# Performance work log

Measured on AMD Instinct MI355X. Metric: run time of the kernel, lower is better.

The kernel has to match this reference:

```python
import jax, jax.numpy as jnp
import numpy as np
from math import factorial, sqrt

LMAX = 2
NB = 32
NRBF = 20
CUTOFF = 5.0
N_ATOMS = 20000
N_EDGES = 400000
T = 2
M = (LMAX + 1) ** 2
LIDX = np.repeat(np.arange(LMAX + 1), 2 * np.arange(LMAX + 1) + 1)  # l of each flat (l,m) index


def _cg_complex(j1, m1, j2, m2, j3, m3):
    # Racah formula for complex-SH Clebsch-Gordan coefficients
    if m3 != m1 + m2 or j3 < abs(j1 - j2) or j3 > j1 + j2:
        return 0.0
    f = factorial
    pref = sqrt((2 * j3 + 1) * f(j1 + j2 - j3) * f(j1 - j2 + j3) * f(-j1 + j2 + j3) / f(j1 + j2 + j3 + 1))
    pref *= sqrt(f(j1 + m1) * f(j1 - m1) * f(j2 + m2) * f(j2 - m2) * f(j3 + m3) * f(j3 - m3))
    kmin = max(0, j2 - j3 - m1, j1 + m2 - j3)
    kmax = min(j1 + j2 - j3, j1 - m1, j2 + m2)
    s = 0.0
    for k in range(kmin, kmax + 1):
        s += (-1) ** k / (f(k) * f(j1 + j2 - j3 - k) * f(j1 - m1 - k) * f(j2 + m2 - k) * f(j3 - j2 + m1 + k) * f(j3 - j1 - m2 + k))
    return pref * s


def _u_matrix(l):
    # real-SH = U @ complex-SH (rows: real m from -l..l, cols: complex m')
    U = np.zeros((2 * l + 1, 2 * l + 1), dtype=np.complex128)
    for m in range(-l, l + 1):
        if m == 0:
            U[l, l] = 1.0
        elif m > 0:
            U[l + m, l + m] = (-1) ** m / sqrt(2)
            U[l + m, l - m] = 1.0 / sqrt(2)
        else:
            mu = -m
            U[l + m, l + m] = 1j / sqrt(2)
            U[l + m, l - m] = -1j * (-1) ** mu / sqrt(2)
    return U


def _build_cg_rsh(lmax):
    # CG coefficients in the real-SH basis, parity invariant (odd l1+l2+l3 blocks zero)
    cg = np.zeros((M, M, M), dtype=np.float64)
    Us = [_u_matrix(l) for l in range(lmax + 1)]
    for l1 in range(lmax + 1):
        for l2 in range(lmax + 1):
            for l3 in range(lmax + 1):
                if (l1 + l2 + l3) % 2 == 1 or l3 < abs(l1 - l2) or l3 > l1 + l2:
                    continue
                Cc = np.zeros((2 * l1 + 1, 2 * l2 + 1, 2 * l3 + 1), dtype=np.complex128)
                for i, m1 in enumerate(range(-l1, l1 + 1)):
                    for j, m2 in enumerate(range(-l2, l2 + 1)):
                        m3 = m1 + m2
                        if abs(m3) <= l3:
                            Cc[i, j, l3 + m3] = _cg_complex(l1, m1, l2, m2, l3, m3)
                R = np.einsum('ai,bj,ck,ijk->abc', Us[l1], Us[l2], np.conj(Us[l3]), Cc)
                cg[l1 * l1:(l1 + 1) ** 2, l2 * l2:(l2 + 1) ** 2, l3 * l3:(l3 + 1) ** 2] = np.real(R)
    return cg.astype(np.float32)


CG = jnp.asarray(_build_cg_rsh(LMAX))   # [9, 9, 9]
LIDX_J = jnp.asarray(LIDX)


def _rsh(dirs):
    # real spherical harmonics up to l=2 on unit vectors, flat (l,m) order -> [P, 9]
    x, y, z = dirs[:, 0], dirs[:, 1], dirs[:, 2]
    c1 = 0.4886025119029199
    c2 = 1.0925484305920792
    return jnp.stack([
        jnp.full_like(x, 0.28209479177387814),
        c1 * y, c1 * z, c1 * x,
        c2 * x * y, c2 * y * z,
        0.31539156525252005 * (3.0 * z * z - 1.0),
        c2 * x * z,
        0.5462742152960396 * (x * x - y * y),
    ], axis=1)


def _forward(atomic_numbers, r_ij, idx_i, idx_j, emb, Wf, bf, Wm1, Wm2, Wm3, Wg, bg):
    d = jnp.linalg.norm(r_ij, axis=1)                      # [P]
    Y = _rsh(r_ij / d[:, None])                            # [P, 9]
    offsets = jnp.linspace(0.0, CUTOFF, NRBF)
    width = CUTOFF / (NRBF - 1)
    radial = jnp.exp(-0.5 / width ** 2 * (d[:, None] - offsets) ** 2)   # GaussianRBF [P, NRBF]
    fcut = jnp.where(d < CUTOFF, 0.5 * (jnp.cos(d * jnp.pi / CUTOFF) + 1.0), 0.0)  # CosineCutoff
    x0 = emb[atomic_numbers]                               # nuclear embedding [N, NB]
    x = jnp.concatenate([x0[:, None, :], jnp.zeros((x0.shape[0], M - 1, NB), x0.dtype)], axis=1)  # scalar2rsh
    for t in range(T):
        # SO3Convolution: per-edge radial filter per output degree l, cutoff gated
        Wl = ((radial @ Wf[t].T + bf[t]) * fcut[:, None]).reshape(-1, LMAX + 1, NB)
        xj = x[idx_j]                                      # gather neighbors [P, 9, NB]
        tbc = jnp.einsum('pa,abc->pbc', Y, CG)             # contract Y_ij with CG
        yij = jnp.einsum('pbc,pbn->pcn', tbc, xj) * Wl[:, LIDX_J, :]
        dx = jax.ops.segment_sum(yij, idx_i, num_segments=x.shape[0], indices_are_sorted=True)
        ddx = jnp.einsum('xcn,kn->xck', dx, Wm1[t])        # mixing1 (no bias)
        dx = dx + jnp.einsum('abc,xan,xbn->xcn', CG, dx, ddx)  # SO3TensorProduct
        dx = jnp.einsum('xcn,kn->xck', dx, Wm2[t])         # mixing2
        h = jax.nn.sigmoid((dx[:, 0, :] @ Wg[t].T + bg[t]).reshape(-1, LMAX + 1, NB))
        dx = dx * h[:, LIDX_J, :]                          # SO3ParametricGatedNonlinearity
        dx = jnp.einsum('xcn,kn->xck', dx, Wm3[t])         # mixing3
        x = x + dx
    return x                                               # multipole representation [N, 9, NB]


def setup_inputs():
    key = jax.random.key(0)
    ks = jax.random.split(key, 12)
    return {
        'atomic_numbers': jax.random.randint(ks[0], (N_ATOMS,), 1, 100),
        'r_ij': jax.random.normal(ks[1], (N_EDGES, 3), jnp.float32),
        'idx_i': jnp.sort(jax.random.randint(ks[2], (N_EDGES,), 0, N_ATOMS)),
        'idx_j': jax.random.randint(ks[3], (N_EDGES,), 0, N_ATOMS),
        'emb': jax.random.normal(ks[4], (101, NB), jnp.float32).at[0].set(0.0),
        'Wf': jax.random.normal(ks[5], (T, (LMAX + 1) * NB, NRBF), jnp.float32) / sqrt(NRBF),
        'bf': jnp.zeros((T, (LMAX + 1) * NB), jnp.float32),
        'Wm1': jax.random.normal(ks[6], (T, NB, NB), jnp.float32) / sqrt(NB),
        'Wm2': jax.random.normal(ks[7], (T, NB, NB), jnp.float32) / sqrt(NB),
        'Wm3': jax.random.normal(ks[8], (T, NB, NB), jnp.float32) / sqrt(NB),
        'Wg': jax.random.normal(ks[9], (T, (LMAX + 1) * NB, NB), jnp.float32) / sqrt(NB),
        'bg': jnp.zeros((T, (LMAX + 1) * NB), jnp.float32),
    }


def reference(atomic_numbers, r_ij, idx_i, idx_j, emb, Wf, bf, Wm1, Wm2, Wm3, Wg, bg):
    return _forward(atomic_numbers, r_ij, idx_i, idx_j, emb, Wf, bf, Wm1, Wm2, Wm3, Wg, bg)
```

## Files before the change

kernel.cpp:

```cpp
#include <hip/hip_runtime.h>

#define CHUNK 16

constexpr double CFACT[8] = {1.,1.,2.,6.,24.,120.,720.,5040.};

constexpr double csqrt(double x){
  if (x <= 0.0) return 0.0;
  double s = 1.0;
  while (x > 4.0)  { x *= 0.25; s *= 2.0; }
  while (x < 0.25) { x *= 4.0;  s *= 0.5; }
  double g = 1.0;
  for (int i=0;i<10;i++) g = 0.5*(g + x/g);
  return s*g;
}

constexpr double cg_complex(int j1,int m1,int j2,int m2,int j3,int m3){
  if (m3 != m1+m2 || j3 < (j1>j2?j1-j2:j2-j1) || j3 > j1+j2) return 0.0;
  double pref = csqrt((2.0*j3+1.0)*CFACT[j1+j2-j3]*CFACT[j1-j2+j3]*CFACT[-j1+j2+j3]/CFACT[j1+j2+j3+1]);
  pref *= csqrt(CFACT[j1+m1]*CFACT[j1-m1]*CFACT[j2+m2]*CFACT[j2-m2]*CFACT[j3+m3]*CFACT[j3-m3]);
  int kmin = 0;
  if (j2-j3-m1 > kmin) kmin = j2-j3-m1;
  if (j1+m2-j3 > kmin) kmin = j1+m2-j3;
  int kmax = j1+j2-j3;
  if (j1-m1 < kmax) kmax = j1-m1;
  if (j2+m2 < kmax) kmax = j2+m2;
  double s = 0.0;
  for (int k=kmin;k<=kmax;++k){
    double t = 1.0/(CFACT[k]*CFACT[j1+j2-j3-k]*CFACT[j1-m1-k]*CFACT[j2+m2-k]*CFACT[j3-j2+m1+k]*CFACT[j3-j1-m2+k]);
    s += (k&1)? -t : t;
  }
  return pref*s;
}

struct UR { int n; int mc[2]; double re[2]; double im[2]; };
constexpr UR u_row(int m){
  UR u{}; const double is2 = 0.70710678118654752440;
  if (m==0){ u.n=1; u.mc[0]=0; u.re[0]=1.0; u.im[0]=0.0; u.mc[1]=0; u.re[1]=0.0; u.im[1]=0.0; }
  else if (m>0){ u.n=2; u.mc[0]=m;  u.re[0]=((m&1)? -is2:is2); u.im[0]=0.0;
                        u.mc[1]=-m; u.re[1]=is2;               u.im[1]=0.0; }
  else { int mu=-m; u.n=2; u.mc[0]=m;  u.re[0]=0.0; u.im[0]=is2;
                           u.mc[1]=mu; u.re[1]=0.0; u.im[1]=((mu&1)? is2:-is2); }
  return u;
}

struct CGTab { float v[9][9][9]; };
constexpr CGTab build_cg(){
  CGTab g{};
  double cc[9][9][9] = {};
  for (int a=0;a<9;a++){
    int l1 = (a==0)?0:((a<4)?1:2); int m1 = a - (l1*l1+l1);
    for (int b=0;b<9;b++){
      int l2 = (b==0)?0:((b<4)?1:2); int m2 = b - (l2*l2+l2);
      int m3 = m1+m2;
      for (int l3=0;l3<=2;l3++){
        if (m3 < -l3 || m3 > l3) continue;
        cc[a][b][l3*l3+l3+m3] = cg_complex(l1,m1,l2,m2,l3,m3);
      }
    }
  }
  for (int l1=0;l1<=2;l1++) for (int l2=0;l2<=2;l2++) for (int l3=0;l3<=2;l3++){
    if (((l1+l2+l3)&1)==1) continue;
    int dl = (l1>l2)?(l1-l2):(l2-l1);
    if (l3 < dl || l3 > l1+l2) continue;
    for (int m1=-l1;m1<=l1;m1++) for (int m2=-l2;m2<=l2;m2++) for (int m3=-l3;m3<=l3;m3++){
      UR ua = u_row(m1), ub = u_row(m2), uc = u_row(m3);
      double acc = 0.0;
      for (int i=0;i<ua.n;i++) for (int j=0;j<ub.n;j++){
        double zr = ua.re[i]*ub.re[j] - ua.im[i]*ub.im[j];
        double zi = ua.re[i]*ub.im[j] + ua.im[i]*ub.re[j];
        for (int k=0;k<uc.n;k++){
          double rp = zr*uc.re[k] + zi*uc.im[k];
          if (rp != 0.0)
            acc += rp * cc[l1*l1+l1+ua.mc[i]][l2*l2+l2+ub.mc[j]][l3*l3+l3+uc.mc[k]];
        }
      }
      g.v[l1*l1+l1+m1][l2*l2+l2+m2][l3*l3+l3+m3] = (float)acc;
    }
  }
  return g;
}
constexpr CGTab CGT = build_cg();

__global__ void init_x_kernel(const int* __restrict__ Z, const float* __restrict__ emb,
                              float4* __restrict__ x4, float4* __restrict__ dx4, int n_atoms){
  int i = blockIdx.x*blockDim.x + threadIdx.x;
  if (i >= n_atoms*72) return;
  int atom = i/72, rem = i - atom*72;
  float4 v = make_float4(0.f,0.f,0.f,0.f);
  if (rem < 8) v = reinterpret_cast<const float4*>(emb)[Z[atom]*8 + rem];
  x4[i] = v;
  dx4[i] = make_float4(0.f,0.f,0.f,0.f);
}

template<bool FIRST>
__global__ __launch_bounds__(256) void edge_kernel(
    const float* __restrict__ r_ij, const int* __restrict__ idx_i, const int* __restrict__ idx_j,
    const float* __restrict__ x, const float* __restrict__ Wf_t, const float* __restrict__ bf_t,
    float* __restrict__ dx, int n_edges)
{
  __shared__ __align__(16) float rbs[8][32];
  int tid = threadIdx.x;
  int g = tid >> 5, lane = tid & 31;
  int base = (blockIdx.x*8 + g)*CHUNK;
  if (base >= n_edges) return;
  const int nend = n_edges;

  float wfr[3][20]; float bfl[3];
  #pragma unroll
  for (int l=0;l<3;l++){
    const float* rp = Wf_t + (l*32+lane)*20;
    #pragma unroll
    for (int q=0;q<5;q++){
      float4 v4 = *reinterpret_cast<const float4*>(rp + q*4);
      wfr[l][q*4+0]=v4.x; wfr[l][q*4+1]=v4.y; wfr[l][q*4+2]=v4.z; wfr[l][q*4+3]=v4.w;
    }
    bfl[l] = bf_t[l*32+lane];
  }

  const float STEP  = 5.0f/19.0f;
  const float ALPHA = -0.5f/(STEP*STEP);
  float myoff = (float)lane * STEP;

  float racc[9];
  #pragma unroll
  for (int c=0;c<9;c++) racc[c]=0.f;
  int cur_i = -1;

  float xj[9]; float xj0 = 0.f;
  {
    int j0 = idx_j[base];
    const float* xp = x + j0*288 + lane;
    if (FIRST){ xj0 = xp[0]; }
    else {
      #pragma unroll
      for (int b=0;b<9;b++) xj[b] = xp[b*32];
    }
  }
  int e1 = (base+1 <= nend-1) ? base+1 : nend-1;
  int j_next = idx_j[e1];

  #pragma unroll 2
  for (int k=0;k<CHUNK;k++){
    int e = base + k;
    if (e >= nend) break;

    float xjn[9]; float xjn0 = 0.f;
    {
      const float* xp = x + j_next*288 + lane;
      if (FIRST){ xjn0 = xp[0]; }
      else {
        #pragma unroll
        for (int b=0;b<9;b++) xjn[b] = xp[b*32];
      }
    }
    int en2 = (e+2 <= nend-1) ? e+2 : nend-1;
    int j_n2 = idx_j[en2];

    int   ii = idx_i[e];
    float rx = r_ij[3*e+0], ry = r_ij[3*e+1], rz = r_ij[3*e+2];

    float d2 = fmaf(rx,rx,fmaf(ry,ry,rz*rz));
    float inv = __frsqrt_rn(d2);
    float dd = d2*inv;
    float X = rx*inv, Yv = ry*inv, Zv = rz*inv;
    const float c1 = 0.4886025119029199f, c2 = 1.0925484305920792f;
    float Y[9];
    Y[0]=0.28209479177387814f; Y[1]=c1*Yv; Y[2]=c1*Zv; Y[3]=c1*X;
    Y[4]=c2*X*Yv; Y[5]=c2*Yv*Zv; Y[6]=0.31539156525252005f*(3.f*Zv*Zv-1.f);
    Y[7]=c2*X*Zv; Y[8]=0.5462742152960396f*(X*X-Yv*Yv);

    float dtl = dd - myoff;
    float rbl = __expf(ALPHA*dtl*dtl);
    if (lane < 20) rbs[g][lane] = rbl;
    __builtin_amdgcn_wave_barrier();
    float rbv[20];
    {
      const float4* rb4 = reinterpret_cast<const float4*>(&rbs[g][0]);
      #pragma unroll
      for (int q=0;q<5;q++){
        float4 v4 = rb4[q];
        rbv[4*q+0]=v4.x; rbv[4*q+1]=v4.y; rbv[4*q+2]=v4.z; rbv[4*q+3]=v4.w;
      }
    }
    float wl0=bfl[0], wl1=bfl[1], wl2=bfl[2];
    #pragma unroll
    for (int r=0;r<20;r++){
      wl0 = fmaf(rbv[r], wfr[0][r], wl0);
      wl1 = fmaf(rbv[r], wfr[1][r], wl1);
      wl2 = fmaf(rbv[r], wfr[2][r], wl2);
    }
    float fc = (dd < 5.0f) ? 0.5f*(__cosf(dd*0.6283185307179586f)+1.0f) : 0.0f;
    wl0*=fc; wl1*=fc; wl2*=fc;

    if (ii != cur_i){
      if (cur_i >= 0){
        float* dp = dx + cur_i*288 + lane;
        #pragma unroll
        for (int c=0;c<9;c++){ atomicAdd(dp + c*32, racc[c]); racc[c]=0.f; }
      }
      cur_i = ii;
    }

    if (FIRST){
      racc[0] = fmaf(wl0, Y[0]*xj0, racc[0]);
      #pragma unroll
      for (int c=1;c<4;c++) racc[c] = fmaf(wl1, Y[c]*xj0, racc[c]);
      #pragma unroll
      for (int c=4;c<9;c++) racc[c] = fmaf(wl2, Y[c]*xj0, racc[c]);
    } else {
      float yv[9];
      #pragma unroll
      for (int c=0;c<9;c++) yv[c]=0.f;
      #pragma unroll
      for (int a=0;a<9;a++){
        #pragma unroll
        for (int b=0;b<9;b++){
          bool any = false;
          #pragma unroll
          for (int c=0;c<9;c++) any = any | (CGT.v[a][b][c] != 0.f);
          if (any){
            float p = Y[a]*xj[b];
            #pragma unroll
            for (int c=0;c<9;c++){
              if (CGT.v[a][b][c] != 0.f) yv[c] = fmaf(CGT.v[a][b][c], p, yv[c]);
            }
          }
        }
      }
      racc[0] = fmaf(wl0, yv[0], racc[0]);
      #pragma unroll
      for (int c=1;c<4;c++) racc[c] = fmaf(wl1, yv[c], racc[c]);
      #pragma unroll
      for (int c=4;c<9;c++) racc[c] = fmaf(wl2, yv[c], racc[c]);
    }

    j_next = j_n2;
    if (FIRST){ xj0 = xjn0; }
    else {
      #pragma unroll
      for (int b=0;b<9;b++) xj[b] = xjn[b];
    }
  }
  if (cur_i >= 0){
    float* dp = dx + cur_i*288 + lane;
    #pragma unroll
    for (int c=0;c<9;c++) atomicAdd(dp + c*32, racc[c]);
  }
}

__global__ __launch_bounds__(256) void atom_kernel(
    float* __restrict__ x, float* __restrict__ dxg,
    const float* __restrict__ Wm1_t, const float* __restrict__ Wm2_t, const float* __restrict__ Wm3_t,
    const float* __restrict__ Wg_t, const float* __restrict__ bg_t, int n_atoms)
{
  __shared__ __align__(16) float tile[8][288];
  int tid = threadIdx.x;
  int g = tid>>5, k = tid&31;
  int atom = blockIdx.x*8 + g;
  if (atom >= n_atoms) return;
  float* tg = &tile[g][0];
  const float4* t4 = reinterpret_cast<const float4*>(tg);

  float* dp = dxg + atom*288 + k;
  float v[9];
  #pragma unroll
  for (int c=0;c<9;c++){ v[c]=dp[c*32]; tg[c*32+k]=v[c]; dp[c*32]=0.f; }

  float wr[32];
  {
    const float4* w4 = reinterpret_cast<const float4*>(Wm1_t + k*32);
    #pragma unroll
    for (int q=0;q<8;q++){ float4 a=w4[q]; wr[4*q]=a.x; wr[4*q+1]=a.y; wr[4*q+2]=a.z; wr[4*q+3]=a.w; }
  }
  float u[9];
  #pragma unroll
  for (int c=0;c<9;c++){
    float s=0.f;
    #pragma unroll
    for (int q=0;q<8;q++){
      float4 tv = t4[c*8+q];
      s = fmaf(tv.x, wr[4*q+0], s); s = fmaf(tv.y, wr[4*q+1], s);
      s = fmaf(tv.z, wr[4*q+2], s); s = fmaf(tv.w, wr[4*q+3], s);
    }
    u[c]=s;
  }

  float w[9];
  #pragma unroll
  for (int c=0;c<9;c++) w[c]=v[c];
  #pragma unroll
  for (int a=0;a<9;a++){
    #pragma unroll
    for (int b=0;b<9;b++){
      bool any = false;
      #pragma unroll
      for (int c=0;c<9;c++) any = any | (CGT.v[a][b][c] != 0.f);
      if (any){
        float p = v[a]*u[b];
        #pragma unroll
        for (int c=0;c<9;c++){
          if (CGT.v[a][b][c] != 0.f) w[c] = fmaf(CGT.v[a][b][c], p, w[c]);
        }
      }
    }
  }

  #pragma unroll
  for (int c=0;c<9;c++) tg[c*32+k]=w[c];
  {
    const float4* w4 = reinterpret_cast<const float4*>(Wm2_t + k*32);
    #pragma unroll
    for (int q=0;q<8;q++){ float4 a=w4[q]; wr[4*q]=a.x; wr[4*q+1]=a.y; wr[4*q+2]=a.z; wr[4*q+3]=a.w; }
  }
  float p[9];
  #pragma unroll
  for (int c=0;c<9;c++){
    float s=0.f;
    #pragma unroll
    for (int q=0;q<8;q++){
      float4 tv = t4[c*8+q];
      s = fmaf(tv.x, wr[4*q+0], s); s = fmaf(tv.y, wr[4*q+1], s);
      s = fmaf(tv.z, wr[4*q+2], s); s = fmaf(tv.w, wr[4*q+3], s);
    }
    p[c]=s;
  }

  tg[k] = p[0];
  float s0=bg_t[k], s1=bg_t[32+k], s2=bg_t[64+k];
  {
    const float4* wg0 = reinterpret_cast<const float4*>(Wg_t + (     k)*32);
    const float4* wg1 = reinterpret_cast<const float4*>(Wg_t + (32 + k)*32);
    const float4* wg2 = reinterpret_cast<const float4*>(Wg_t + (64 + k)*32);
    #pragma unroll
    for (int q=0;q<8;q++){
      float4 tv = t4[q];
      float4 a0 = wg0[q], a1 = wg1[q], a2 = wg2[q];
      s0 = fmaf(tv.x,a0.x,s0); s0 = fmaf(tv.y,a0.y,s0); s0 = fmaf(tv.z,a0.z,s0); s0 = fmaf(tv.w,a0.w,s0);
      s1 = fmaf(tv.x,a1.x,s1); s1 = fmaf(tv.y,a1.y,s1); s1 = fmaf(tv.z,a1.z,s1); s1 = fmaf(tv.w,a1.w,s1);
      s2 = fmaf(tv.x,a2.x,s2); s2 = fmaf(tv.y,a2.y,s2); s2 = fmaf(tv.z,a2.z,s2); s2 = fmaf(tv.w,a2.w,s2);
    }
  }
  float h0 = 1.f/(1.f+__expf(-s0));
  float h1 = 1.f/(1.f+__expf(-s1));
  float h2 = 1.f/(1.f+__expf(-s2));

  float q9[9];
  q9[0]=p[0]*h0;
  #pragma unroll
  for (int c=1;c<4;c++) q9[c]=p[c]*h1;
  #pragma unroll
  for (int c=4;c<9;c++) q9[c]=p[c]*h2;

  #pragma unroll
  for (int c=0;c<9;c++) tg[c*32+k]=q9[c];
  {
    const float4* w4 = reinterpret_cast<const float4*>(Wm3_t + k*32);
    #pragma unroll
    for (int q=0;q<8;q++){ float4 a=w4[q]; wr[4*q]=a.x; wr[4*q+1]=a.y; wr[4*q+2]=a.z; wr[4*q+3]=a.w; }
  }
  float* xo = x + atom*288 + k;
  #pragma unroll
  for (int c=0;c<9;c++){
    float s=0.f;
    #pragma unroll
    for (int q=0;q<8;q++){
      float4 tv = t4[c*8+q];
      s = fmaf(tv.x, wr[4*q+0], s); s = fmaf(tv.y, wr[4*q+1], s);
      s = fmaf(tv.z, wr[4*q+2], s); s = fmaf(tv.w, wr[4*q+3], s);
    }
    xo[c*32] += s;
  }
}

extern "C" void kernel_launch(void* const* d_in, const int* in_sizes, int n_in,
                              void* d_out, int out_size, void* d_ws, size_t ws_size,
                              hipStream_t stream)
{
  const int*   Z    = (const int*)d_in[0];
  const float* r_ij = (const float*)d_in[1];
  const int*   idxi = (const int*)d_in[2];
  const int*   idxj = (const int*)d_in[3];
  const float* emb  = (const float*)d_in[4];
  const float* Wf   = (const float*)d_in[5];
  const float* bf   = (const float*)d_in[6];
  const float* Wm1  = (const float*)d_in[7];
  const float* Wm2  = (const float*)d_in[8];
  const float* Wm3  = (const float*)d_in[9];
  const float* Wg   = (const float*)d_in[10];
  const float* bg   = (const float*)d_in[11];
  int n_atoms = in_sizes[0];
  int n_edges = in_sizes[1]/3;

  float* x  = (float*)d_out;
  float* dx = (float*)d_ws;

  init_x_kernel<<<(n_atoms*72+255)/256,256,0,stream>>>(Z, emb, (float4*)x, (float4*)dx, n_atoms);

  int eblocks = (n_edges + 8*CHUNK - 1)/(8*CHUNK);
  int ablocks = (n_atoms + 7)/8;

  edge_kernel<true><<<eblocks,256,0,stream>>>(r_ij, idxi, idxj, x, Wf, bf, dx, n_edges);
  atom_kernel<<<ablocks,256,0,stream>>>(x, dx, Wm1, Wm2, Wm3, Wg, bg, n_atoms);

  edge_kernel<false><<<eblocks,256,0,stream>>>(r_ij, idxi, idxj, x,
                                        Wf + 96*20, bf + 96, dx, n_edges);
  atom_kernel<<<ablocks,256,0,stream>>>(x, dx,
                                        Wm1 + 1024, Wm2 + 1024, Wm3 + 1024,
                                        Wg + 96*32, bg + 96, n_atoms);
}
```

Measured before the change: 385.0 us.

## Use packed FMA for radial filter and deepen FIRST-layer gather prefetch

Stores the radial filter weights as float2 pairs and computes the three filter dot products with packed elementwise FMAs, intended to lower to v_pk_fma_f32 and halve the FMA instruction count. In the FIRST edge kernel, the x_j gather prefetch is extended to two edges ahead to hide more load latency. The distance is now computed with sqrtf instead of d2*rsqrt, which costs an extra instruction but avoids a NaN for zero-length vectors. Pairwise accumulation reorders the float sums slightly, and the deeper prefetch keeps more registers live.

```diff
diff --git a/kernel.cpp b/kernel.cpp
--- a/kernel.cpp
+++ b/kernel.cpp
@@ -1,6 +1,8 @@
 #include <hip/hip_runtime.h>
 
 #define CHUNK 16
+
+typedef float f32x2 __attribute__((ext_vector_type(2)));
 
 constexpr double CFACT[8] = {1.,1.,2.,6.,24.,120.,720.,5040.};
 
@@ -105,14 +107,15 @@
   if (base >= n_edges) return;
   const int nend = n_edges;
 
-  float wfr[3][20]; float bfl[3];
+  f32x2 wfp[3][10]; float bfl[3];
   #pragma unroll
   for (int l=0;l<3;l++){
     const float* rp = Wf_t + (l*32+lane)*20;
     #pragma unroll
     for (int q=0;q<5;q++){
       float4 v4 = *reinterpret_cast<const float4*>(rp + q*4);
-      wfr[l][q*4+0]=v4.x; wfr[l][q*4+1]=v4.y; wfr[l][q*4+2]=v4.z; wfr[l][q*4+3]=v4.w;
+      wfp[l][2*q]   = f32x2{v4.x, v4.y};
+      wfp[l][2*q+1] = f32x2{v4.z, v4.w};
     }
     bfl[l] = bf_t[l*32+lane];
   }
@@ -126,7 +129,8 @@
   for (int c=0;c<9;c++) racc[c]=0.f;
   int cur_i = -1;
 
-  float xj[9]; float xj0 = 0.f;
+  float xj[9]; float xj0 = 0.f, xj0_n = 0.f;
+  int j_next, j_next2 = 0;
   {
     int j0 = idx_j[base];
     const float* xp = x + j0*288 + lane;
@@ -135,33 +139,40 @@
       #pragma unroll
       for (int b=0;b<9;b++) xj[b] = xp[b*32];
     }
-  }
-  int e1 = (base+1 <= nend-1) ? base+1 : nend-1;
-  int j_next = idx_j[e1];
+    int e1 = (base+1 <= nend-1) ? base+1 : nend-1;
+    j_next = idx_j[e1];
+    if (FIRST){
+      xj0_n = x[j_next*288 + lane];
+      int e2 = (base+2 <= nend-1) ? base+2 : nend-1;
+      j_next2 = idx_j[e2];
+    }
+  }
 
   #pragma unroll 2
   for (int k=0;k<CHUNK;k++){
     int e = base + k;
     if (e >= nend) break;
 
-    float xjn[9]; float xjn0 = 0.f;
-    {
+    float xjn[9]; float xj0_n2 = 0.f;
+    int j_n2;
+    if (FIRST){
+      xj0_n2 = x[j_next2*288 + lane];
+      int e3 = (e+3 <= nend-1) ? e+3 : nend-1;
+      j_n2 = idx_j[e3];
+    } else {
       const float* xp = x + j_next*288 + lane;
-      if (FIRST){ xjn0 = xp[0]; }
-      else {
-        #pragma unroll
-        for (int b=0;b<9;b++) xjn[b] = xp[b*32];
-      }
-    }
-    int en2 = (e+2 <= nend-1) ? e+2 : nend-1;
-    int j_n2 = idx_j[en2];
+      #pragma unroll
+      for (int b=0;b<9;b++) xjn[b] = xp[b*32];
+      int en2 = (e+2 <= nend-1) ? e+2 : nend-1;
+      j_n2 = idx_j[en2];
+    }
 
     int   ii = idx_i[e];
     float rx = r_ij[3*e+0], ry = r_ij[3*e+1], rz = r_ij[3*e+2];
 
     float d2 = fmaf(rx,rx,fmaf(ry,ry,rz*rz));
     float inv = __frsqrt_rn(d2);
-    float dd = d2*inv;
+    float dd = sqrtf(d2);
     float X = rx*inv, Yv = ry*inv, Zv = rz*inv;
     const float c1 = 0.4886025119029199f, c2 = 1.0925484305920792f;
     float Y[9];
@@ -173,24 +184,28 @@
     float rbl = __expf(ALPHA*dtl*dtl);
     if (lane < 20) rbs[g][lane] = rbl;
     __builtin_amdgcn_wave_barrier();
-    float rbv[20];
+    f32x2 a0 = f32x2{bfl[0], 0.f};
+    f32x2 a1 = f32x2{bfl[1], 0.f};
+    f32x2 a2 = f32x2{bfl[2], 0.f};
     {
       const float4* rb4 = reinterpret_cast<const float4*>(&rbs[g][0]);
       #pragma unroll
       for (int q=0;q<5;q++){
         float4 v4 = rb4[q];
-        rbv[4*q+0]=v4.x; rbv[4*q+1]=v4.y; rbv[4*q+2]=v4.z; rbv[4*q+3]=v4.w;
-      }
-    }
-    float wl0=bfl[0], wl1=bfl[1], wl2=bfl[2];
-    #pragma unroll
-    for (int r=0;r<20;r++){
-      wl0 = fmaf(rbv[r], wfr[0][r], wl0);
-      wl1 = fmaf(rbv[r], wfr[1][r], wl1);
-      wl2 = fmaf(rbv[r], wfr[2][r], wl2);
+        f32x2 ra = f32x2{v4.x, v4.y};
+        f32x2 rb = f32x2{v4.z, v4.w};
+        a0 = __builtin_elementwise_fma(ra, wfp[0][2*q],   a0);
+        a1 = __builtin_elementwise_fma(ra, wfp[1][2*q],   a1);
+        a2 = __builtin_elementwise_fma(ra, wfp[2][2*q],   a2);
+        a0 = __builtin_elementwise_fma(rb, wfp[0][2*q+1], a0);
+        a1 = __builtin_elementwise_fma(rb, wfp[1][2*q+1], a1);
+        a2 = __builtin_elementwise_fma(rb, wfp[2][2*q+1], a2);
+      }
     }
     float fc = (dd < 5.0f) ? 0.5f*(__cosf(dd*0.6283185307179586f)+1.0f) : 0.0f;
-    wl0*=fc; wl1*=fc; wl2*=fc;
+    float wl0 = (a0.x + a0.y)*fc;
+    float wl1 = (a1.x + a1.y)*fc;
+    float wl2 = (a2.x + a2.y)*fc;
 
     if (ii != cur_i){
       if (cur_i >= 0){
@@ -234,11 +249,13 @@
       for (int c=4;c<9;c++) racc[c] = fmaf(wl2, yv[c], racc[c]);
     }
 
-    j_next = j_n2;
-    if (FIRST){ xj0 = xjn0; }
-    else {
+    if (FIRST){
+      xj0 = xj0_n; xj0_n = xj0_n2;
+      j_next2 = j_n2;
+    } else {
       #pragma unroll
       for (int b=0;b<9;b++) xj[b] = xjn[b];
+      j_next = j_n2;
     }
   }
   if (cur_i >= 0){
```

Measured after the change: 385.1 us. About the same (+0.0%).

## Halve edge chunk size and specialize edge loop for in-bounds chunks

Applied to the files above, without the earlier changes.

Halves CHUNK from 16 to 8, so twice as many wavefronts are launched over the edges. The edge loop moves into a templated device function with a CLAMP flag, and chunks that lie fully in bounds run without the per-iteration clamp and break checks. It also computes distance with sqrtf instead of d2*rsqrt, and removes the lane<20 guard on the shared-memory store. More chunks means more per-wave setup: Wf register loads and extra atomic flushes at chunk boundaries.

```diff
diff --git a/kernel.cpp b/kernel.cpp
--- a/kernel.cpp
+++ b/kernel.cpp
@@ -1,6 +1,6 @@
 #include <hip/hip_runtime.h>
 
-#define CHUNK 16
+#define CHUNK 8
 
 constexpr double CFACT[8] = {1.,1.,2.,6.,24.,120.,720.,5040.};
 
@@ -92,34 +92,16 @@
   dx4[i] = make_float4(0.f,0.f,0.f,0.f);
 }
 
-template<bool FIRST>
-__global__ __launch_bounds__(256) void edge_kernel(
-    const float* __restrict__ r_ij, const int* __restrict__ idx_i, const int* __restrict__ idx_j,
-    const float* __restrict__ x, const float* __restrict__ Wf_t, const float* __restrict__ bf_t,
-    float* __restrict__ dx, int n_edges)
+template<bool FIRST, bool CLAMP>
+__device__ __forceinline__ void edge_loop(
+    int base, int nend, int lane, float* __restrict__ rbsg,
+    const float* __restrict__ r_ij, const int* __restrict__ idx_i,
+    const int* __restrict__ idx_j, const float* __restrict__ x,
+    const float (&wfr)[3][20], const float (&bfl)[3], float myoff,
+    float* __restrict__ dx)
 {
-  __shared__ __align__(16) float rbs[8][32];
-  int tid = threadIdx.x;
-  int g = tid >> 5, lane = tid & 31;
-  int base = (blockIdx.x*8 + g)*CHUNK;
-  if (base >= n_edges) return;
-  const int nend = n_edges;
-
-  float wfr[3][20]; float bfl[3];
-  #pragma unroll
-  for (int l=0;l<3;l++){
-    const float* rp = Wf_t + (l*32+lane)*20;
-    #pragma unroll
-    for (int q=0;q<5;q++){
-      float4 v4 = *reinterpret_cast<const float4*>(rp + q*4);
-      wfr[l][q*4+0]=v4.x; wfr[l][q*4+1]=v4.y; wfr[l][q*4+2]=v4.z; wfr[l][q*4+3]=v4.w;
-    }
-    bfl[l] = bf_t[l*32+lane];
-  }
-
   const float STEP  = 5.0f/19.0f;
   const float ALPHA = -0.5f/(STEP*STEP);
-  float myoff = (float)lane * STEP;
 
   float racc[9];
   #pragma unroll
@@ -136,13 +118,14 @@
       for (int b=0;b<9;b++) xj[b] = xp[b*32];
     }
   }
-  int e1 = (base+1 <= nend-1) ? base+1 : nend-1;
+  int e1 = base+1;
+  if (CLAMP && e1 > nend-1) e1 = nend-1;
   int j_next = idx_j[e1];
 
   #pragma unroll 2
   for (int k=0;k<CHUNK;k++){
     int e = base + k;
-    if (e >= nend) break;
+    if (CLAMP && e >= nend) break;
 
     float xjn[9]; float xjn0 = 0.f;
     {
@@ -153,7 +136,8 @@
         for (int b=0;b<9;b++) xjn[b] = xp[b*32];
       }
     }
-    int en2 = (e+2 <= nend-1) ? e+2 : nend-1;
+    int en2 = e+2;
+    if (CLAMP && en2 > nend-1) en2 = nend-1;
     int j_n2 = idx_j[en2];
 
     int   ii = idx_i[e];
@@ -161,7 +145,7 @@
 
     float d2 = fmaf(rx,rx,fmaf(ry,ry,rz*rz));
     float inv = __frsqrt_rn(d2);
-    float dd = d2*inv;
+    float dd = sqrtf(d2);
     float X = rx*inv, Yv = ry*inv, Zv = rz*inv;
     const float c1 = 0.4886025119029199f, c2 = 1.0925484305920792f;
     float Y[9];
@@ -171,11 +155,11 @@
 
     float dtl = dd - myoff;
     float rbl = __expf(ALPHA*dtl*dtl);
-    if (lane < 20) rbs[g][lane] = rbl;
+    rbsg[lane] = rbl;
     __builtin_amdgcn_wave_barrier();
     float rbv[20];
     {
-      const float4* rb4 = reinterpret_cast<const float4*>(&rbs[g][0]);
+      const float4* rb4 = reinterpret_cast<const float4*>(rbsg);
       #pragma unroll
       for (int q=0;q<5;q++){
         float4 v4 = rb4[q];
@@ -245,6 +229,41 @@
     float* dp = dx + cur_i*288 + lane;
     #pragma unroll
     for (int c=0;c<9;c++) atomicAdd(dp + c*32, racc[c]);
+  }
+}
+
+template<bool FIRST>
+__global__ __launch_bounds__(256) void edge_kernel(
+    const float* __restrict__ r_ij, const int* __restrict__ idx_i, const int* __restrict__ idx_j,
+    const float* __restrict__ x, const float* __restrict__ Wf_t, const float* __restrict__ bf_t,
+    float* __restrict__ dx, int n_edges)
+{
+  __shared__ __align__(16) float rbs[8][32];
+  int tid = threadIdx.x;
+  int g = tid >> 5, lane = tid & 31;
+  int base = (blockIdx.x*8 + g)*CHUNK;
+  if (base >= n_edges) return;
+
+  float wfr[3][20]; float bfl[3];
+  #pragma unroll
+  for (int l=0;l<3;l++){
+    const float* rp = Wf_t + (l*32+lane)*20;
+    #pragma unroll
+    for (int q=0;q<5;q++){
+      float4 v4 = *reinterpret_cast<const float4*>(rp + q*4);
+      wfr[l][q*4+0]=v4.x; wfr[l][q*4+1]=v4.y; wfr[l][q*4+2]=v4.z; wfr[l][q*4+3]=v4.w;
+    }
+    bfl[l] = bf_t[l*32+lane];
+  }
+  const float STEP = 5.0f/19.0f;
+  float myoff = (float)lane * STEP;
+
+  if (base + CHUNK + 2 <= n_edges){
+    edge_loop<FIRST,false>(base, n_edges, lane, &rbs[g][0],
+                           r_ij, idx_i, idx_j, x, wfr, bfl, myoff, dx);
+  } else {
+    edge_loop<FIRST,true>(base, n_edges, lane, &rbs[g][0],
+                          r_ij, idx_i, idx_j, x, wfr, bfl, myoff, dx);
   }
 }
 
```

New measurement: 484.6 us. +25.9%, slower.

## Fold x init into kernels, use readlane matvecs instead of LDS tiles

Applied to the files above, without the earlier changes.

Removes the init_x kernel: the first edge pass reads embeddings directly via Z/emb, the first atom pass writes x fresh as emb plus update, and dx is zeroed with a memset. The atom kernel now maps one atom per 64-lane wave (lanes 32-63 duplicate) and does its 32x32 matvecs with readlane broadcasts instead of shared-memory tiles. It also switches dd to sqrtf and lets all lanes write the rbf scratch. This trades one kernel launch and the x/dx traffic for duplicated work in half of each wave and many scalar readlane ops.

```diff
diff --git a/kernel.cpp b/kernel.cpp
--- a/kernel.cpp
+++ b/kernel.cpp
@@ -81,21 +81,11 @@
 }
 constexpr CGTab CGT = build_cg();
 
-__global__ void init_x_kernel(const int* __restrict__ Z, const float* __restrict__ emb,
-                              float4* __restrict__ x4, float4* __restrict__ dx4, int n_atoms){
-  int i = blockIdx.x*blockDim.x + threadIdx.x;
-  if (i >= n_atoms*72) return;
-  int atom = i/72, rem = i - atom*72;
-  float4 v = make_float4(0.f,0.f,0.f,0.f);
-  if (rem < 8) v = reinterpret_cast<const float4*>(emb)[Z[atom]*8 + rem];
-  x4[i] = v;
-  dx4[i] = make_float4(0.f,0.f,0.f,0.f);
-}
-
 template<bool FIRST>
 __global__ __launch_bounds__(256) void edge_kernel(
     const float* __restrict__ r_ij, const int* __restrict__ idx_i, const int* __restrict__ idx_j,
-    const float* __restrict__ x, const float* __restrict__ Wf_t, const float* __restrict__ bf_t,
+    const float* __restrict__ x, const int* __restrict__ Z, const float* __restrict__ emb,
+    const float* __restrict__ Wf_t, const float* __restrict__ bf_t,
     float* __restrict__ dx, int n_edges)
 {
   __shared__ __align__(16) float rbs[8][32];
@@ -127,17 +117,19 @@
   int cur_i = -1;
 
   float xj[9]; float xj0 = 0.f;
+  int zn = 0;
   {
     int j0 = idx_j[base];
-    const float* xp = x + j0*288 + lane;
-    if (FIRST){ xj0 = xp[0]; }
+    if (FIRST){ xj0 = emb[Z[j0]*32 + lane]; }
     else {
+      const float* xp = x + j0*288 + lane;
       #pragma unroll
       for (int b=0;b<9;b++) xj[b] = xp[b*32];
     }
   }
   int e1 = (base+1 <= nend-1) ? base+1 : nend-1;
   int j_next = idx_j[e1];
+  if (FIRST) zn = Z[j_next];
 
   #pragma unroll 2
   for (int k=0;k<CHUNK;k++){
@@ -145,23 +137,24 @@
     if (e >= nend) break;
 
     float xjn[9]; float xjn0 = 0.f;
-    {
+    if (FIRST){
+      xjn0 = emb[zn*32 + lane];
+    } else {
       const float* xp = x + j_next*288 + lane;
-      if (FIRST){ xjn0 = xp[0]; }
-      else {
-        #pragma unroll
-        for (int b=0;b<9;b++) xjn[b] = xp[b*32];
-      }
+      #pragma unroll
+      for (int b=0;b<9;b++) xjn[b] = xp[b*32];
     }
     int en2 = (e+2 <= nend-1) ? e+2 : nend-1;
     int j_n2 = idx_j[en2];
+    int zn2 = 0;
+    if (FIRST) zn2 = Z[j_n2];
 
     int   ii = idx_i[e];
     float rx = r_ij[3*e+0], ry = r_ij[3*e+1], rz = r_ij[3*e+2];
 
     float d2 = fmaf(rx,rx,fmaf(ry,ry,rz*rz));
     float inv = __frsqrt_rn(d2);
-    float dd = d2*inv;
+    float dd = sqrtf(d2);
     float X = rx*inv, Yv = ry*inv, Zv = rz*inv;
     const float c1 = 0.4886025119029199f, c2 = 1.0925484305920792f;
     float Y[9];
@@ -171,7 +164,7 @@
 
     float dtl = dd - myoff;
     float rbl = __expf(ALPHA*dtl*dtl);
-    if (lane < 20) rbs[g][lane] = rbl;
+    rbs[g][lane] = rbl;
     __builtin_amdgcn_wave_barrier();
     float rbv[20];
     {
@@ -235,7 +228,7 @@
     }
 
     j_next = j_n2;
-    if (FIRST){ xj0 = xjn0; }
+    if (FIRST){ xj0 = xjn0; zn = zn2; }
     else {
       #pragma unroll
       for (int b=0;b<9;b++) xj[b] = xjn[b];
@@ -248,46 +241,47 @@
   }
 }
 
+__device__ __forceinline__ float rl(float v, int n){
+  return __int_as_float(__builtin_amdgcn_readlane(__float_as_int(v), n));
+}
+__device__ __forceinline__ void load_row(const float* __restrict__ W, int k, float (&wr)[32]){
+  const float4* w4 = reinterpret_cast<const float4*>(W + k*32);
+  #pragma unroll
+  for (int q=0;q<8;q++){ float4 a=w4[q]; wr[4*q]=a.x; wr[4*q+1]=a.y; wr[4*q+2]=a.z; wr[4*q+3]=a.w; }
+}
+
+template<bool FIRST_T>
 __global__ __launch_bounds__(256) void atom_kernel(
     float* __restrict__ x, float* __restrict__ dxg,
+    const int* __restrict__ Z, const float* __restrict__ emb,
     const float* __restrict__ Wm1_t, const float* __restrict__ Wm2_t, const float* __restrict__ Wm3_t,
     const float* __restrict__ Wg_t, const float* __restrict__ bg_t, int n_atoms)
 {
-  __shared__ __align__(16) float tile[8][288];
   int tid = threadIdx.x;
-  int g = tid>>5, k = tid&31;
-  int atom = blockIdx.x*8 + g;
+  int wv = tid >> 6, lane = tid & 63, k = lane & 31;
+  int atom = blockIdx.x*4 + wv;
   if (atom >= n_atoms) return;
-  float* tg = &tile[g][0];
-  const float4* t4 = reinterpret_cast<const float4*>(tg);
 
   float* dp = dxg + atom*288 + k;
   float v[9];
   #pragma unroll
-  for (int c=0;c<9;c++){ v[c]=dp[c*32]; tg[c*32+k]=v[c]; dp[c*32]=0.f; }
+  for (int c=0;c<9;c++){ v[c]=dp[c*32]; dp[c*32]=0.f; }
 
   float wr[32];
-  {
-    const float4* w4 = reinterpret_cast<const float4*>(Wm1_t + k*32);
-    #pragma unroll
-    for (int q=0;q<8;q++){ float4 a=w4[q]; wr[4*q]=a.x; wr[4*q+1]=a.y; wr[4*q+2]=a.z; wr[4*q+3]=a.w; }
-  }
+
+  load_row(Wm1_t, k, wr);
   float u[9];
   #pragma unroll
   for (int c=0;c<9;c++){
     float s=0.f;
     #pragma unroll
-    for (int q=0;q<8;q++){
-      float4 tv = t4[c*8+q];
-      s = fmaf(tv.x, wr[4*q+0], s); s = fmaf(tv.y, wr[4*q+1], s);
-      s = fmaf(tv.z, wr[4*q+2], s); s = fmaf(tv.w, wr[4*q+3], s);
-    }
+    for (int n=0;n<32;n++) s = fmaf(rl(v[c],n), wr[n], s);
     u[c]=s;
   }
 
-  float w[9];
-  #pragma unroll
-  for (int c=0;c<9;c++) w[c]=v[c];
+  float w9[9];
+  #pragma unroll
+  for (int c=0;c<9;c++) w9[c]=v[c];
   #pragma unroll
   for (int a=0;a<9;a++){
     #pragma unroll
@@ -299,76 +293,53 @@
         float p = v[a]*u[b];
         #pragma unroll
         for (int c=0;c<9;c++){
-          if (CGT.v[a][b][c] != 0.f) w[c] = fmaf(CGT.v[a][b][c], p, w[c]);
+          if (CGT.v[a][b][c] != 0.f) w9[c] = fmaf(CGT.v[a][b][c], p, w9[c]);
         }
       }
     }
   }
 
-  #pragma unroll
-  for (int c=0;c<9;c++) tg[c*32+k]=w[c];
-  {
-    const float4* w4 = reinterpret_cast<const float4*>(Wm2_t + k*32);
-    #pragma unroll
-    for (int q=0;q<8;q++){ float4 a=w4[q]; wr[4*q]=a.x; wr[4*q+1]=a.y; wr[4*q+2]=a.z; wr[4*q+3]=a.w; }
-  }
+  load_row(Wm2_t, k, wr);
   float p[9];
   #pragma unroll
   for (int c=0;c<9;c++){
     float s=0.f;
     #pragma unroll
-    for (int q=0;q<8;q++){
-      float4 tv = t4[c*8+q];
-      s = fmaf(tv.x, wr[4*q+0], s); s = fmaf(tv.y, wr[4*q+1], s);
-      s = fmaf(tv.z, wr[4*q+2], s); s = fmaf(tv.w, wr[4*q+3], s);
-    }
+    for (int n=0;n<32;n++) s = fmaf(rl(w9[c],n), wr[n], s);
     p[c]=s;
   }
 
-  tg[k] = p[0];
-  float s0=bg_t[k], s1=bg_t[32+k], s2=bg_t[64+k];
-  {
-    const float4* wg0 = reinterpret_cast<const float4*>(Wg_t + (     k)*32);
-    const float4* wg1 = reinterpret_cast<const float4*>(Wg_t + (32 + k)*32);
-    const float4* wg2 = reinterpret_cast<const float4*>(Wg_t + (64 + k)*32);
-    #pragma unroll
-    for (int q=0;q<8;q++){
-      float4 tv = t4[q];
-      float4 a0 = wg0[q], a1 = wg1[q], a2 = wg2[q];
-      s0 = fmaf(tv.x,a0.x,s0); s0 = fmaf(tv.y,a0.y,s0); s0 = fmaf(tv.z,a0.z,s0); s0 = fmaf(tv.w,a0.w,s0);
-      s1 = fmaf(tv.x,a1.x,s1); s1 = fmaf(tv.y,a1.y,s1); s1 = fmaf(tv.z,a1.z,s1); s1 = fmaf(tv.w,a1.w,s1);
-      s2 = fmaf(tv.x,a2.x,s2); s2 = fmaf(tv.y,a2.y,s2); s2 = fmaf(tv.z,a2.z,s2); s2 = fmaf(tv.w,a2.w,s2);
-    }
-  }
-  float h0 = 1.f/(1.f+__expf(-s0));
-  float h1 = 1.f/(1.f+__expf(-s1));
-  float h2 = 1.f/(1.f+__expf(-s2));
+  float p0 = p[0];
+  float h[3];
+  #pragma unroll
+  for (int l=0;l<3;l++){
+    load_row(Wg_t, l*32 + k, wr);
+    float s = bg_t[l*32 + k];
+    #pragma unroll
+    for (int n=0;n<32;n++) s = fmaf(rl(p0,n), wr[n], s);
+    h[l] = 1.f/(1.f+__expf(-s));
+  }
 
   float q9[9];
-  q9[0]=p[0]*h0;
-  #pragma unroll
-  for (int c=1;c<4;c++) q9[c]=p[c]*h1;
-  #pragma unroll
-  for (int c=4;c<9;c++) q9[c]=p[c]*h2;
-
-  #pragma unroll
-  for (int c=0;c<9;c++) tg[c*32+k]=q9[c];
-  {
-    const float4* w4 = reinterpret_cast<const float4*>(Wm3_t + k*32);
-    #pragma unroll
-    for (int q=0;q<8;q++){ float4 a=w4[q]; wr[4*q]=a.x; wr[4*q+1]=a.y; wr[4*q+2]=a.z; wr[4*q+3]=a.w; }
-  }
+  q9[0]=p[0]*h[0];
+  #pragma unroll
+  for (int c=1;c<4;c++) q9[c]=p[c]*h[1];
+  #pragma unroll
+  for (int c=4;c<9;c++) q9[c]=p[c]*h[2];
+
+  load_row(Wm3_t, k, wr);
   float* xo = x + atom*288 + k;
   #pragma unroll
   for (int c=0;c<9;c++){
     float s=0.f;
     #pragma unroll
-    for (int q=0;q<8;q++){
-      float4 tv = t4[c*8+q];
-      s = fmaf(tv.x, wr[4*q+0], s); s = fmaf(tv.y, wr[4*q+1], s);
-      s = fmaf(tv.z, wr[4*q+2], s); s = fmaf(tv.w, wr[4*q+3], s);
-    }
-    xo[c*32] += s;
+    for (int n=0;n<32;n++) s = fmaf(rl(q9[c],n), wr[n], s);
+    if (FIRST_T){
+      float init = (c==0) ? emb[Z[atom]*32 + k] : 0.f;
+      xo[c*32] = init + s;
+    } else {
+      xo[c*32] += s;
+    }
   }
 }
 
@@ -394,17 +365,17 @@
   float* x  = (float*)d_out;
   float* dx = (float*)d_ws;
 
-  init_x_kernel<<<(n_atoms*72+255)/256,256,0,stream>>>(Z, emb, (float4*)x, (float4*)dx, n_atoms);
+  hipMemsetAsync(dx, 0, (size_t)n_atoms*288*sizeof(float), stream);
 
   int eblocks = (n_edges + 8*CHUNK - 1)/(8*CHUNK);
-  int ablocks = (n_atoms + 7)/8;
-
-  edge_kernel<true><<<eblocks,256,0,stream>>>(r_ij, idxi, idxj, x, Wf, bf, dx, n_edges);
-  atom_kernel<<<ablocks,256,0,stream>>>(x, dx, Wm1, Wm2, Wm3, Wg, bg, n_atoms);
-
-  edge_kernel<false><<<eblocks,256,0,stream>>>(r_ij, idxi, idxj, x,
+  int ablocks = (n_atoms + 3)/4;
+
+  edge_kernel<true><<<eblocks,256,0,stream>>>(r_ij, idxi, idxj, x, Z, emb, Wf, bf, dx, n_edges);
+  atom_kernel<true><<<ablocks,256,0,stream>>>(x, dx, Z, emb, Wm1, Wm2, Wm3, Wg, bg, n_atoms);
+
+  edge_kernel<false><<<eblocks,256,0,stream>>>(r_ij, idxi, idxj, x, Z, emb,
                                         Wf + 96*20, bf + 96, dx, n_edges);
-  atom_kernel<<<ablocks,256,0,stream>>>(x, dx,
+  atom_kernel<false><<<ablocks,256,0,stream>>>(x, dx, Z, emb,
                                         Wm1 + 1024, Wm2 + 1024, Wm3 + 1024,
                                         Wg + 96*32, bg + 96, n_atoms);
 }
```

After: 491.1 us. 1.28x slower.
